# Performance work log

Hardware: AMD Instinct MI355X
Metric: run time of the kernel (lower is better)

## Reference

```python
import jax, jax.numpy as jnp
import numpy as np

B, N, F_IN, F_OUT = 8, 4096, 256, 256


def setup_inputs() -> dict:
    key = jax.random.key(0)
    k1, k2, k3 = jax.random.split(key, 3)
    H = jax.random.normal(k1, (B, N, F_IN), dtype=jnp.float32)
    W = jax.random.normal(k2, (F_IN, F_OUT), dtype=jnp.float32) * (1.0 / np.sqrt(F_IN))
    A = jax.random.normal(k3, (N, N), dtype=jnp.float32) * (1.414 * np.sqrt(2.0 / (N + N)))
    return {"H": H, "W": W, "A": A}


def reference(H, W, A):
    # HW: [B, N, F_out]
    HW = jnp.einsum('bnf,fo->bno', H, W)
    # symmetrize + relu -> nonneg adjacency [N, N]
    A_norm = jax.nn.relu((A + A.T) * 0.5)
    # degree and inverse sqrt (inf -> 0 for isolated nodes)
    D = jnp.sum(A_norm, axis=1)
    D_safe = jnp.where(D > 0, D, 1.0)
    d_inv_sqrt = jnp.where(D > 0, D_safe ** -0.5, 0.0)
    # L_norm = I - D^{-1/2} A D^{-1/2}  (diagonal scaling, no dense diag matmul)
    DAD = d_inv_sqrt[:, None] * A_norm * d_inv_sqrt[None, :]
    L_norm = jnp.eye(N, dtype=H.dtype) - DAD
    # output = relu(L_norm @ HW): [B, N, F_out]
    out = jnp.einsum('nm,bmo->bno', L_norm, HW)
    return jax.nn.relu(out)
```

## Files before the change

### kernel.cpp

```cpp
#include <hip/hip_runtime.h>
#include <stdint.h>

#define N_NODES 4096
#define F_DIM   256
#define BATCH   8

typedef __attribute__((ext_vector_type(8))) __bf16 bf16x8;
typedef __attribute__((ext_vector_type(4))) float  f32x4;
typedef __attribute__((ext_vector_type(8))) unsigned short u16x8;

typedef const __attribute__((address_space(1))) void* gas1_t;
typedef __attribute__((address_space(3))) void*       las3_t;

__device__ __forceinline__ void stage16(const void* g, void* l) {
  __builtin_amdgcn_global_load_lds((gas1_t)g, (las3_t)l, 16, 0, 0);
}

__device__ __forceinline__ unsigned short f2bf(float f) {
  union { float f; uint32_t u; } v; v.f = f;
  uint32_t u = v.u;
  return (unsigned short)((u + 0x7FFFu + ((u >> 16) & 1u)) >> 16);
}
__device__ __forceinline__ float bf2f(unsigned short u) {
  union { uint32_t u; float f; } v; v.u = ((uint32_t)u) << 16;
  return v.f;
}

__global__ __launch_bounds__(256) void k_pre(const float* __restrict__ A,
                                             unsigned short* __restrict__ Sb,
                                             float* __restrict__ D,
                                             const float4* __restrict__ H4,
                                             ushort4* __restrict__ Hb4,
                                             const float* __restrict__ W,
                                             unsigned short* __restrict__ Wt) {
  int t = threadIdx.x;
  int bid = blockIdx.y * 64 + blockIdx.x;
  {
    int i = bid * 512 + t;
    float4 v = H4[i];
    ushort4 o; o.x = f2bf(v.x); o.y = f2bf(v.y); o.z = f2bf(v.z); o.w = f2bf(v.w);
    Hb4[i] = o;
    i += 256;
    v = H4[i];
    o.x = f2bf(v.x); o.y = f2bf(v.y); o.z = f2bf(v.z); o.w = f2bf(v.w);
    Hb4[i] = o;
  }
  if (bid < 256) Wt[t * 256 + bid] = f2bf(W[bid * 256 + t]);

  int bi = blockIdx.y, bj = blockIdx.x;
  if (bj < bi) return;

  __shared__ __align__(16) float T1[64][68];
  __shared__ float Tt[64][67];
  __shared__ float Pr4[64][4];
  __shared__ float Pc[4][64];
  int i0 = bi * 64, j0 = bj * 64;

#pragma unroll
  for (int it = 0; it < 4; ++it) {
    int idx = it * 256 + t;
    int r = idx >> 4, c4 = (idx & 15) * 4;
    float4 v1 = *(const float4*)(A + (size_t)(i0 + r) * N_NODES + j0 + c4);
    *(float4*)&T1[r][c4] = v1;
    float4 v2 = *(const float4*)(A + (size_t)(j0 + r) * N_NODES + i0 + c4);
    Tt[c4 + 0][r] = v2.x; Tt[c4 + 1][r] = v2.y; Tt[c4 + 2][r] = v2.z; Tt[c4 + 3][r] = v2.w;
  }
  __syncthreads();

  {
    int r = t >> 2, cb = (t & 3) * 8;
    float rowpart = 0.f;
#pragma unroll
    for (int g = 0; g < 2; ++g) {
      int c0 = cb + g * 32;
      u16x8 u;
      float vv[8];
#pragma unroll
      for (int i = 0; i < 8; ++i) {
        float v = 0.5f * (T1[r][c0 + i] + Tt[r][c0 + i]);
        v = v > 0.f ? v : 0.f;
        vv[i] = v;
        rowpart += v;
        u[i] = f2bf(v);
      }
      *(u16x8*)&Sb[(size_t)(i0 + r) * N_NODES + j0 + c0] = u;
      *(float4*)&T1[r][c0]     = make_float4(vv[0], vv[1], vv[2], vv[3]);
      *(float4*)&T1[r][c0 + 4] = make_float4(vv[4], vv[5], vv[6], vv[7]);
    }
    Pr4[r][t & 3] = rowpart;
  }
  __syncthreads();

  {
    int c = t & 63, seg = t >> 6;
    float s = 0.f;
#pragma unroll
    for (int i = 0; i < 16; ++i) s += T1[seg * 16 + i][c];
    Pc[seg][c] = s;
  }
  __syncthreads();

  if (t < 64) {
    atomicAdd(&D[i0 + t], Pr4[t][0] + Pr4[t][1] + Pr4[t][2] + Pr4[t][3]);
  } else if (t < 128 && bi != bj) {
    int c = t - 64;
    atomicAdd(&D[j0 + c], Pc[0][c] + Pc[1][c] + Pc[2][c] + Pc[3][c]);
  }

  if (bi != bj) {
#pragma unroll
    for (int it = 0; it < 2; ++it) {
      int u = it * 256 + t;
      int co = u >> 3, rc = (u & 7) * 8;
      u16x8 o;
#pragma unroll
      for (int i = 0; i < 8; ++i) o[i] = f2bf(T1[rc + i][co]);
      *(u16x8*)&Sb[(size_t)(j0 + co) * N_NODES + i0 + rc] = o;
    }
  }
}

__global__ void k_dinv(const float* __restrict__ D, float* __restrict__ dinv) {
  int i = blockIdx.x * blockDim.x + threadIdx.x;
  if (i < N_NODES) {
    float d = D[i];
    dinv[i] = d > 0.f ? 1.0f / sqrtf(d) : 0.f;
  }
}

__global__ __launch_bounds__(512) void k_gemm1(const unsigned short* __restrict__ Hb,
                                               const unsigned short* __restrict__ Wt,
                                               const float* __restrict__ dinv,
                                               unsigned short* __restrict__ HWb,
                                               unsigned short* __restrict__ Gt) {
  __shared__ __align__(16) unsigned short L[65536];
  int t = threadIdx.x;
  int lane = t & 63, r16 = lane & 15, q = lane >> 4;
  int wave = t >> 6;
  int wm = wave >> 2, wn = wave & 3;
  int nh = blockIdx.x;
  int m0 = blockIdx.y * 128;
  int n0 = nh * 128;

#pragma unroll
  for (int i = 0; i < 8; ++i) {
    int s = i * 512 + t;
    int row = s >> 5, cl = s & 31;
    int cs = cl ^ (row & 7);
    uint32_t dst = (uint32_t)(i * 512 + (t & ~63)) * 16;
    stage16(Hb + (size_t)(m0 + row) * 256 + cs * 8, (char*)L + dst);
    stage16(Wt + (size_t)(n0 + row) * 256 + cs * 8, (char*)L + 65536 + dst);
  }
  __syncthreads();

  f32x4 acc[4][2];
#pragma unroll
  for (int i = 0; i < 4; ++i)
#pragma unroll
    for (int j = 0; j < 2; ++j) acc[i][j] = f32x4{0.f, 0.f, 0.f, 0.f};

#pragma unroll
  for (int ks = 0; ks < 8; ++ks) {
    bf16x8 a[4], b[2];
#pragma unroll
    for (int mi = 0; mi < 4; ++mi) {
      int ra = wm * 64 + mi * 16 + r16;
      a[mi] = *(const bf16x8*)((const char*)L + ra * 512 + (((ks * 4 + q) ^ (ra & 7)) << 4));
    }
#pragma unroll
    for (int ni = 0; ni < 2; ++ni) {
      int rb = wn * 32 + ni * 16 + r16;
      b[ni] = *(const bf16x8*)((const char*)L + 65536 + rb * 512 + (((ks * 4 + q) ^ (rb & 7)) << 4));
    }
#pragma unroll
    for (int mi = 0; mi < 4; ++mi)
#pragma unroll
      for (int ni = 0; ni < 2; ++ni)
        acc[mi][ni] = __builtin_amdgcn_mfma_f32_16x16x32_bf16(a[mi], b[ni], acc[mi][ni], 0, 0, 0);
  }
  __syncthreads();

  unsigned short (*T)[136] = (unsigned short (*)[136])L;
#pragma unroll
  for (int mi = 0; mi < 4; ++mi) {
    int rowl = wm * 64 + mi * 16 + q * 4;
#pragma unroll
    for (int ni = 0; ni < 2; ++ni) {
      int coll = wn * 32 + ni * 16 + r16;
#pragma unroll
      for (int rr = 0; rr < 4; ++rr) {
        unsigned short h = f2bf(acc[mi][ni][rr]);
        HWb[(size_t)(m0 + rowl + rr) * F_DIM + (n0 + coll)] = h;
        T[coll][rowl + rr] = h;
      }
    }
  }
  __syncthreads();

  int b = m0 >> 12, nb = m0 & 4095;
#pragma unroll
  for (int i = 0; i < 4; ++i) {
    int u = i * 512 + t;
    int co = u >> 4, cs = (u & 15) * 8;
    u16x8 v = *(const u16x8*)&T[co][cs];
    float4 d0 = *(const float4*)&dinv[nb + cs];
    float4 d1 = *(const float4*)&dinv[nb + cs + 4];
    u16x8 w;
    w[0] = f2bf(bf2f(v[0]) * d0.x);
    w[1] = f2bf(bf2f(v[1]) * d0.y);
    w[2] = f2bf(bf2f(v[2]) * d0.z);
    w[3] = f2bf(bf2f(v[3]) * d0.w);
    w[4] = f2bf(bf2f(v[4]) * d1.x);
    w[5] = f2bf(bf2f(v[5]) * d1.y);
    w[6] = f2bf(bf2f(v[6]) * d1.z);
    w[7] = f2bf(bf2f(v[7]) * d1.w);
    *(u16x8*)&Gt[(size_t)(b * 256 + n0 + co) * N_NODES + nb + cs] = w;
  }
}

#define LDSB 49152

__global__ __launch_bounds__(512, 2) void k_gemm2(const unsigned short* __restrict__ Sb,
                                                  const unsigned short* __restrict__ Gt,
                                                  const unsigned short* __restrict__ HWb,
                                                  const float* __restrict__ dinv,
                                                  float* __restrict__ Out) {
  __shared__ __align__(16) unsigned short LDS[3 * 24576];
  const int NT = N_NODES / 64;
  int t = threadIdx.x;
  int lane = t & 63, r16 = lane & 15, q = lane >> 4;
  int wave = t >> 6;
  int wm = wave >> 1, wn = wave & 1;

  int bid = blockIdx.x;
  int xcd = bid & 7, j = bid >> 3;
  int mt = (xcd >> 1) * 4 + (j & 3);
  int nt = (xcd & 1) * 8 + (j >> 2);
  int m0 = mt * 256, n0 = nt * 128;

  const char* aSrc[4]; const char* bSrc[2];
  uint32_t aDst[4], bDst[2];
#pragma unroll
  for (int i = 0; i < 4; ++i) {
    int slot = i * 512 + t;
    int row = slot >> 3;
    int c = (slot & 7) ^ (row & 7);
    aSrc[i] = (const char*)Sb + (size_t)(m0 + row) * 8192 + c * 16;
    aDst[i] = (uint32_t)(i * 512 + (t & ~63)) * 16;
  }
#pragma unroll
  for (int i = 0; i < 2; ++i) {
    int slot = i * 512 + t;
    int row = slot >> 3;
    int c = (slot & 7) ^ (row & 7);
    bSrc[i] = (const char*)Gt + (size_t)(n0 + row) * 8192 + c * 16;
    bDst[i] = 32768u + (uint32_t)(i * 512 + (t & ~63)) * 16;
  }

  int aoff[4][2], boff[4][2];
#pragma unroll
  for (int mi = 0; mi < 4; ++mi) {
    int ra = wm * 64 + mi * 16 + r16;
#pragma unroll
    for (int ks = 0; ks < 2; ++ks)
      aoff[mi][ks] = ra * 128 + (((ks * 4 + q) ^ (ra & 7)) << 4);
  }
#pragma unroll
  for (int ni = 0; ni < 4; ++ni) {
    int rb = wn * 64 + ni * 16 + r16;
#pragma unroll
    for (int ks = 0; ks < 2; ++ks)
      boff[ni][ks] = 32768 + rb * 128 + (((ks * 4 + q) ^ (rb & 7)) << 4);
  }

  f32x4 acc[4][4];
#pragma unroll
  for (int i = 0; i < 4; ++i)
#pragma unroll
    for (int jj = 0; jj < 4; ++jj) acc[i][jj] = f32x4{0.f, 0.f, 0.f, 0.f};

  auto stage_tile = [&](int kt2, uint32_t bufByte) {
    size_t kb = (size_t)kt2 * 128;
#pragma unroll
    for (int i = 0; i < 4; ++i)
      stage16(aSrc[i] + kb, (char*)LDS + bufByte + aDst[i]);
#pragma unroll
    for (int i = 0; i < 2; ++i)
      stage16(bSrc[i] + kb, (char*)LDS + bufByte + bDst[i]);
  };

  auto tile_body = [&](int kt, uint32_t cur, int mode) {
    bf16x8 aR[4][2], bR[4][2];
#pragma unroll
    for (int mi = 0; mi < 4; ++mi)
#pragma unroll
      for (int ks = 0; ks < 2; ++ks)
        aR[mi][ks] = *(const bf16x8*)((const char*)LDS + cur + aoff[mi][ks]);
#pragma unroll
    for (int ni = 0; ni < 4; ++ni)
#pragma unroll
      for (int ks = 0; ks < 2; ++ks)
        bR[ni][ks] = *(const bf16x8*)((const char*)LDS + cur + boff[ni][ks]);
    if (mode == 2) {
      uint32_t stg = cur + 2 * LDSB;
      if (stg >= 3 * LDSB) stg -= 3 * LDSB;
      stage_tile(kt + 2, stg);
    }
    __builtin_amdgcn_sched_barrier(0);
    __builtin_amdgcn_s_setprio(1);
#pragma unroll
    for (int ks = 0; ks < 2; ++ks)
#pragma unroll
      for (int mi = 0; mi < 4; ++mi)
#pragma unroll
        for (int ni = 0; ni < 4; ++ni)
          acc[mi][ni] = __builtin_amdgcn_mfma_f32_16x16x32_bf16(aR[mi][ks], bR[ni][ks], acc[mi][ni], 0, 0, 0);
    __builtin_amdgcn_s_setprio(0);
    if (mode == 2) {
      asm volatile("s_waitcnt vmcnt(6)" ::: "memory");
    } else if (mode == 1) {
      asm volatile("s_waitcnt vmcnt(0)" ::: "memory");
    }
    if (mode != 0) {
      __builtin_amdgcn_s_barrier();
      __builtin_amdgcn_sched_barrier(0);
    }
  };

  stage_tile(0, 0);
  stage_tile(1, LDSB);
  asm volatile("s_waitcnt vmcnt(6)" ::: "memory");
  __builtin_amdgcn_s_barrier();
  __builtin_amdgcn_sched_barrier(0);

  uint32_t cur = 0;
#pragma unroll 1
  for (int kt = 0; kt < NT - 2; ++kt) {
    tile_body(kt, cur, 2);
    cur += LDSB; if (cur == 3 * LDSB) cur = 0;
  }
  tile_body(NT - 2, cur, 1);
  cur += LDSB; if (cur == 3 * LDSB) cur = 0;
  tile_body(NT - 1, cur, 0);

  int bq = n0 >> 8;
#pragma unroll
  for (int mi = 0; mi < 4; ++mi) {
    int row = m0 + wm * 64 + mi * 16 + q * 4;
    float di[4];
#pragma unroll
    for (int rr = 0; rr < 4; ++rr) di[rr] = dinv[row + rr];
#pragma unroll
    for (int ni = 0; ni < 4; ++ni) {
      int col = n0 + wn * 64 + ni * 16 + r16;
      int o = col & 255;
#pragma unroll
      for (int rr = 0; rr < 4; ++rr) {
        size_t oi = ((size_t)bq * N_NODES + (row + rr)) * F_DIM + o;
        float u = bf2f(HWb[oi]) - di[rr] * acc[mi][ni][rr];
        Out[oi] = u > 0.f ? u : 0.f;
      }
    }
  }
}

extern "C" void kernel_launch(void* const* d_in, const int* in_sizes, int n_in,
                              void* d_out, int out_size, void* d_ws, size_t ws_size,
                              hipStream_t stream) {
  (void)in_sizes; (void)n_in; (void)out_size; (void)ws_size;
  const float* H = (const float*)d_in[0];
  const float* W = (const float*)d_in[1];
  const float* A = (const float*)d_in[2];
  float* out = (float*)d_out;

  char* ws = (char*)d_ws;
  size_t off = 0;
  auto alloc = [&](size_t bytes) {
    char* p = ws + off;
    off += (bytes + 255) & ~(size_t)255;
    return p;
  };
  float*          Dd   = (float*)alloc((size_t)N_NODES * 4);
  float*          dinv = (float*)alloc((size_t)N_NODES * 4);
  unsigned short* Sb   = (unsigned short*)alloc((size_t)N_NODES * N_NODES * 2);
  unsigned short* HWb  = (unsigned short*)alloc((size_t)BATCH * N_NODES * F_DIM * 2);
  unsigned short* Gt   = (unsigned short*)alloc((size_t)BATCH * F_DIM * N_NODES * 2);
  unsigned short* Wt   = (unsigned short*)alloc((size_t)F_DIM * F_DIM * 2);
  unsigned short* Hb   = (unsigned short*)alloc((size_t)BATCH * N_NODES * F_DIM * 2);

  hipMemsetAsync(Dd, 0, N_NODES * 4, stream);
  k_pre<<<dim3(64, 64), 256, 0, stream>>>(A, Sb, Dd, (const float4*)H, (ushort4*)Hb, W, Wt);
  k_dinv<<<16, 256, 0, stream>>>(Dd, dinv);
  k_gemm1<<<dim3(2, 256), 512, 0, stream>>>(Hb, Wt, dinv, HWb, Gt);
  k_gemm2<<<dim3(256), 512, 0, stream>>>(Sb, Gt, HWb, dinv, out);
}
```

Before: 220.1 us.

## Fuse all stages into one cooperative persistent kernel with grid syncs

Merges the preprocessing, degree/dinv, first GEMM and main GEMM kernels into a single cooperative kernel of 256 blocks separated by grid.sync barriers. This removes three kernel launches and the memset. Degree accumulation now writes per-tile partial sums to a buffer and reduces them deterministically instead of using atomics. The triangular A tiles are spread across blocks with a grid-stride loop. The costs are reduced parallelism in the preprocessing phases (256 blocks instead of thousands) and grid-barrier overhead, and the block count relies on two blocks fitting per CU.

New measurement: 322.1 us. 46.3% more time.

```diff
diff --git a/kernel.cpp b/kernel.cpp
--- a/kernel.cpp
+++ b/kernel.cpp
@@ -1,5 +1,9 @@
 #include <hip/hip_runtime.h>
+#include <hip/hip_cooperative_groups.h>
 #include <stdint.h>
+#include <math.h>
+
+namespace cg = cooperative_groups;
 
 #define N_NODES 4096
 #define F_DIM   256
@@ -25,340 +29,323 @@
   union { uint32_t u; float f; } v; v.u = ((uint32_t)u) << 16;
   return v.f;
 }
-
-__global__ __launch_bounds__(256) void k_pre(const float* __restrict__ A,
-                                             unsigned short* __restrict__ Sb,
-                                             float* __restrict__ D,
-                                             const float4* __restrict__ H4,
-                                             ushort4* __restrict__ Hb4,
-                                             const float* __restrict__ W,
-                                             unsigned short* __restrict__ Wt) {
+__device__ __forceinline__ float dinv_of(float d) {
+  return d > 0.f ? 1.0f / sqrtf(d) : 0.f;
+}
+
+#define LDSB 49152
+
+__global__ __launch_bounds__(512, 2) void k_all(
+    const float* __restrict__ A,
+    const float4* __restrict__ H4,
+    const float* __restrict__ W,
+    unsigned short* __restrict__ Sb,
+    ushort4* __restrict__ Hb4,
+    unsigned short* __restrict__ Wt,
+    float* __restrict__ Dpart,
+    float* __restrict__ dinvA,
+    unsigned short* __restrict__ HWb,
+    unsigned short* __restrict__ Gt,
+    float* __restrict__ Out) {
+  cg::grid_group grid = cg::this_grid();
+  __shared__ __align__(16) unsigned short SMEM[3 * 24576];
+  char* sm = (char*)SMEM;
   int t = threadIdx.x;
-  int bid = blockIdx.y * 64 + blockIdx.x;
-  {
-    int i = bid * 512 + t;
+  int bid = blockIdx.x;
+
+#pragma unroll
+  for (int it = 0; it < 16; ++it) {
+    int i = (bid * 16 + it) * 512 + t;
     float4 v = H4[i];
     ushort4 o; o.x = f2bf(v.x); o.y = f2bf(v.y); o.z = f2bf(v.z); o.w = f2bf(v.w);
     Hb4[i] = o;
-    i += 256;
-    v = H4[i];
-    o.x = f2bf(v.x); o.y = f2bf(v.y); o.z = f2bf(v.z); o.w = f2bf(v.w);
-    Hb4[i] = o;
-  }
-  if (bid < 256) Wt[t * 256 + bid] = f2bf(W[bid * 256 + t]);
-
-  int bi = blockIdx.y, bj = blockIdx.x;
-  if (bj < bi) return;
-
-  __shared__ __align__(16) float T1[64][68];
-  __shared__ float Tt[64][67];
-  __shared__ float Pr4[64][4];
-  __shared__ float Pc[4][64];
-  int i0 = bi * 64, j0 = bj * 64;
-
-#pragma unroll
-  for (int it = 0; it < 4; ++it) {
-    int idx = it * 256 + t;
-    int r = idx >> 4, c4 = (idx & 15) * 4;
-    float4 v1 = *(const float4*)(A + (size_t)(i0 + r) * N_NODES + j0 + c4);
-    *(float4*)&T1[r][c4] = v1;
-    float4 v2 = *(const float4*)(A + (size_t)(j0 + r) * N_NODES + i0 + c4);
-    Tt[c4 + 0][r] = v2.x; Tt[c4 + 1][r] = v2.y; Tt[c4 + 2][r] = v2.z; Tt[c4 + 3][r] = v2.w;
-  }
-  __syncthreads();
+  }
+  if (bid < 128) {
+    int e = bid * 512 + t;
+    Wt[(e & 255) * 256 + (e >> 8)] = f2bf(W[e]);
+  }
 
   {
-    int r = t >> 2, cb = (t & 3) * 8;
-    float rowpart = 0.f;
-#pragma unroll
-    for (int g = 0; g < 2; ++g) {
-      int c0 = cb + g * 32;
+    float (*T1)[68] = (float (*)[68])sm;
+    float (*Tt)[67] = (float (*)[67])(sm + 17408);
+    for (int q = bid; q < 2080; q += 256) {
+      int bi = (int)((129.0 - sqrt(129.0 * 129.0 - 8.0 * (double)q)) * 0.5);
+      while (bi * (129 - bi) / 2 > q) --bi;
+      while ((bi + 1) * (128 - bi) / 2 <= q) ++bi;
+      int bj = bi + (q - bi * (129 - bi) / 2);
+      int i0 = bi * 64, j0 = bj * 64;
+      __syncthreads();
+#pragma unroll
+      for (int it = 0; it < 2; ++it) {
+        int idx = it * 512 + t;
+        int r = idx >> 4, c4 = (idx & 15) * 4;
+        float4 v1 = *(const float4*)(A + (size_t)(i0 + r) * N_NODES + j0 + c4);
+        *(float4*)&T1[r][c4] = v1;
+        float4 v2 = *(const float4*)(A + (size_t)(j0 + r) * N_NODES + i0 + c4);
+        Tt[c4 + 0][r] = v2.x; Tt[c4 + 1][r] = v2.y; Tt[c4 + 2][r] = v2.z; Tt[c4 + 3][r] = v2.w;
+      }
+      __syncthreads();
+      int r = t >> 3, g = t & 7, c0 = g * 8;
+      float vv[8]; float rp = 0.f;
       u16x8 u;
-      float vv[8];
 #pragma unroll
       for (int i = 0; i < 8; ++i) {
         float v = 0.5f * (T1[r][c0 + i] + Tt[r][c0 + i]);
         v = v > 0.f ? v : 0.f;
-        vv[i] = v;
-        rowpart += v;
-        u[i] = f2bf(v);
+        vv[i] = v; rp += v; u[i] = f2bf(v);
       }
       *(u16x8*)&Sb[(size_t)(i0 + r) * N_NODES + j0 + c0] = u;
-      *(float4*)&T1[r][c0]     = make_float4(vv[0], vv[1], vv[2], vv[3]);
-      *(float4*)&T1[r][c0 + 4] = make_float4(vv[4], vv[5], vv[6], vv[7]);
-    }
-    Pr4[r][t & 3] = rowpart;
-  }
-  __syncthreads();
+      rp += __shfl_xor(rp, 1); rp += __shfl_xor(rp, 2); rp += __shfl_xor(rp, 4);
+      if (g == 0) Dpart[(size_t)bj * N_NODES + i0 + r] = rp;
+      if (bi != bj) {
+        __syncthreads();
+#pragma unroll
+        for (int i = 0; i < 8; ++i) Tt[c0 + i][r] = vv[i];
+        __syncthreads();
+        u16x8 o; float cp = 0.f;
+#pragma unroll
+        for (int i = 0; i < 8; ++i) { float x = Tt[r][c0 + i]; o[i] = f2bf(x); cp += x; }
+        *(u16x8*)&Sb[(size_t)(j0 + r) * N_NODES + i0 + c0] = o;
+        cp += __shfl_xor(cp, 1); cp += __shfl_xor(cp, 2); cp += __shfl_xor(cp, 4);
+        if (g == 0) Dpart[(size_t)bi * N_NODES + j0 + r] = cp;
+      }
+    }
+  }
+  grid.sync();
 
   {
-    int c = t & 63, seg = t >> 6;
-    float s = 0.f;
-#pragma unroll
-    for (int i = 0; i < 16; ++i) s += T1[seg * 16 + i][c];
-    Pc[seg][c] = s;
-  }
-  __syncthreads();
-
-  if (t < 64) {
-    atomicAdd(&D[i0 + t], Pr4[t][0] + Pr4[t][1] + Pr4[t][2] + Pr4[t][3]);
-  } else if (t < 128 && bi != bj) {
-    int c = t - 64;
-    atomicAdd(&D[j0 + c], Pc[0][c] + Pc[1][c] + Pc[2][c] + Pc[3][c]);
-  }
-
-  if (bi != bj) {
-#pragma unroll
-    for (int it = 0; it < 2; ++it) {
-      int u = it * 256 + t;
-      int co = u >> 3, rc = (u & 7) * 8;
-      u16x8 o;
-#pragma unroll
-      for (int i = 0; i < 8; ++i) o[i] = f2bf(T1[rc + i][co]);
-      *(u16x8*)&Sb[(size_t)(j0 + co) * N_NODES + i0 + rc] = o;
-    }
-  }
-}
-
-__global__ void k_dinv(const float* __restrict__ D, float* __restrict__ dinv) {
-  int i = blockIdx.x * blockDim.x + threadIdx.x;
-  if (i < N_NODES) {
-    float d = D[i];
-    dinv[i] = d > 0.f ? 1.0f / sqrtf(d) : 0.f;
-  }
-}
-
-__global__ __launch_bounds__(512) void k_gemm1(const unsigned short* __restrict__ Hb,
-                                               const unsigned short* __restrict__ Wt,
-                                               const float* __restrict__ dinv,
-                                               unsigned short* __restrict__ HWb,
-                                               unsigned short* __restrict__ Gt) {
-  __shared__ __align__(16) unsigned short L[65536];
-  int t = threadIdx.x;
-  int lane = t & 63, r16 = lane & 15, q = lane >> 4;
-  int wave = t >> 6;
-  int wm = wave >> 2, wn = wave & 3;
-  int nh = blockIdx.x;
-  int m0 = blockIdx.y * 128;
-  int n0 = nh * 128;
-
-#pragma unroll
-  for (int i = 0; i < 8; ++i) {
-    int s = i * 512 + t;
-    int row = s >> 5, cl = s & 31;
-    int cs = cl ^ (row & 7);
-    uint32_t dst = (uint32_t)(i * 512 + (t & ~63)) * 16;
-    stage16(Hb + (size_t)(m0 + row) * 256 + cs * 8, (char*)L + dst);
-    stage16(Wt + (size_t)(n0 + row) * 256 + cs * 8, (char*)L + 65536 + dst);
-  }
-  __syncthreads();
-
-  f32x4 acc[4][2];
-#pragma unroll
-  for (int i = 0; i < 4; ++i)
-#pragma unroll
-    for (int j = 0; j < 2; ++j) acc[i][j] = f32x4{0.f, 0.f, 0.f, 0.f};
-
-#pragma unroll
-  for (int ks = 0; ks < 8; ++ks) {
-    bf16x8 a[4], b[2];
+    int rl = t >> 5, l32 = t & 31;
+    int row = bid * 16 + rl;
+    float s = Dpart[(size_t)(2 * l32) * N_NODES + row] +
+              Dpart[(size_t)(2 * l32 + 1) * N_NODES + row];
+    s += __shfl_xor(s, 1); s += __shfl_xor(s, 2); s += __shfl_xor(s, 4);
+    s += __shfl_xor(s, 8); s += __shfl_xor(s, 16);
+    if (l32 == 0) dinvA[row] = dinv_of(s);
+  }
+  grid.sync();
+
+  {
+    unsigned short* L = (unsigned short*)sm;
+    int lane = t & 63, r16 = lane & 15, qq = lane >> 4;
+    int wave = t >> 6;
+    int wm = wave >> 2, wn = wave & 3;
+#pragma unroll 1
+    for (int jt = 0; jt < 2; ++jt) {
+      int job = bid + jt * 256;
+      int nh = job & 1, my = job >> 1;
+      int m0 = my * 128, n0 = nh * 128;
+      __syncthreads();
+#pragma unroll
+      for (int i = 0; i < 8; ++i) {
+        int s = i * 512 + t;
+        int row = s >> 5, cl = s & 31;
+        int cs = cl ^ (row & 7);
+        uint32_t dst = (uint32_t)(i * 512 + (t & ~63)) * 16;
+        stage16((const unsigned short*)Hb4 + (size_t)(m0 + row) * 256 + cs * 8, sm + dst);
+        stage16(Wt + (size_t)(n0 + row) * 256 + cs * 8, sm + 65536 + dst);
+      }
+      __syncthreads();
+
+      f32x4 acc[4][2];
+#pragma unroll
+      for (int i = 0; i < 4; ++i)
+#pragma unroll
+        for (int j = 0; j < 2; ++j) acc[i][j] = f32x4{0.f, 0.f, 0.f, 0.f};
+
+#pragma unroll
+      for (int ks = 0; ks < 8; ++ks) {
+        bf16x8 a[4], b[2];
+#pragma unroll
+        for (int mi = 0; mi < 4; ++mi) {
+          int ra = wm * 64 + mi * 16 + r16;
+          a[mi] = *(const bf16x8*)(sm + ra * 512 + (((ks * 4 + qq) ^ (ra & 7)) << 4));
+        }
+#pragma unroll
+        for (int ni = 0; ni < 2; ++ni) {
+          int rb = wn * 32 + ni * 16 + r16;
+          b[ni] = *(const bf16x8*)(sm + 65536 + rb * 512 + (((ks * 4 + qq) ^ (rb & 7)) << 4));
+        }
+#pragma unroll
+        for (int mi = 0; mi < 4; ++mi)
+#pragma unroll
+          for (int ni = 0; ni < 2; ++ni)
+            acc[mi][ni] = __builtin_amdgcn_mfma_f32_16x16x32_bf16(a[mi], b[ni], acc[mi][ni], 0, 0, 0);
+      }
+      __syncthreads();
+
+      unsigned short (*T)[136] = (unsigned short (*)[136])sm;
+#pragma unroll
+      for (int mi = 0; mi < 4; ++mi) {
+        int rowl = wm * 64 + mi * 16 + qq * 4;
+#pragma unroll
+        for (int ni = 0; ni < 2; ++ni) {
+          int coll = wn * 32 + ni * 16 + r16;
+#pragma unroll
+          for (int rr = 0; rr < 4; ++rr) {
+            unsigned short h = f2bf(acc[mi][ni][rr]);
+            HWb[(size_t)(m0 + rowl + rr) * F_DIM + (n0 + coll)] = h;
+            T[coll][rowl + rr] = h;
+          }
+        }
+      }
+      __syncthreads();
+
+      int b = m0 >> 12, nb = m0 & 4095;
+#pragma unroll
+      for (int i = 0; i < 4; ++i) {
+        int u = i * 512 + t;
+        int co = u >> 4, cs = (u & 15) * 8;
+        u16x8 v = *(const u16x8*)&T[co][cs];
+        float4 d0 = *(const float4*)&dinvA[nb + cs];
+        float4 d1 = *(const float4*)&dinvA[nb + cs + 4];
+        u16x8 w;
+        w[0] = f2bf(bf2f(v[0]) * d0.x);
+        w[1] = f2bf(bf2f(v[1]) * d0.y);
+        w[2] = f2bf(bf2f(v[2]) * d0.z);
+        w[3] = f2bf(bf2f(v[3]) * d0.w);
+        w[4] = f2bf(bf2f(v[4]) * d1.x);
+        w[5] = f2bf(bf2f(v[5]) * d1.y);
+        w[6] = f2bf(bf2f(v[6]) * d1.z);
+        w[7] = f2bf(bf2f(v[7]) * d1.w);
+        *(u16x8*)&Gt[(size_t)(b * 256 + n0 + co) * N_NODES + nb + cs] = w;
+      }
+    }
+  }
+  grid.sync();
+
+  {
+    const int NT = N_NODES / 64;
+    int lane = t & 63, r16 = lane & 15, q = lane >> 4;
+    int wave = t >> 6;
+    int wm = wave >> 1, wn = wave & 1;
+
+    int xcd = bid & 7, j = bid >> 3;
+    int mt = (xcd >> 1) * 4 + (j & 3);
+    int nt = (xcd & 1) * 8 + (j >> 2);
+    int m0 = mt * 256, n0 = nt * 128;
+
+    const char* aSrc[4]; const char* bSrc[2];
+    uint32_t aDst[4], bDst[2];
+#pragma unroll
+    for (int i = 0; i < 4; ++i) {
+      int slot = i * 512 + t;
+      int row = slot >> 3;
+      int c = (slot & 7) ^ (row & 7);
+      aSrc[i] = (const char*)Sb + (size_t)(m0 + row) * 8192 + c * 16;
+      aDst[i] = (uint32_t)(i * 512 + (t & ~63)) * 16;
+    }
+#pragma unroll
+    for (int i = 0; i < 2; ++i) {
+      int slot = i * 512 + t;
+      int row = slot >> 3;
+      int c = (slot & 7) ^ (row & 7);
+      bSrc[i] = (const char*)Gt + (size_t)(n0 + row) * 8192 + c * 16;
+      bDst[i] = 32768u + (uint32_t)(i * 512 + (t & ~63)) * 16;
+    }
+
+    int aoff[4][2], boff[4][2];
 #pragma unroll
     for (int mi = 0; mi < 4; ++mi) {
       int ra = wm * 64 + mi * 16 + r16;
-      a[mi] = *(const bf16x8*)((const char*)L + ra * 512 + (((ks * 4 + q) ^ (ra & 7)) << 4));
-    }
-#pragma unroll
-    for (int ni = 0; ni < 2; ++ni) {
-      int rb = wn * 32 + ni * 16 + r16;
-      b[ni] = *(const bf16x8*)((const char*)L + 65536 + rb * 512 + (((ks * 4 + q) ^ (rb & 7)) << 4));
-    }
-#pragma unroll
-    for (int mi = 0; mi < 4; ++mi)
-#pragma unroll
-      for (int ni = 0; ni < 2; ++ni)
-        acc[mi][ni] = __builtin_amdgcn_mfma_f32_16x16x32_bf16(a[mi], b[ni], acc[mi][ni], 0, 0, 0);
-  }
-  __syncthreads();
-
-  unsigned short (*T)[136] = (unsigned short (*)[136])L;
-#pragma unroll
-  for (int mi = 0; mi < 4; ++mi) {
-    int rowl = wm * 64 + mi * 16 + q * 4;
-#pragma unroll
-    for (int ni = 0; ni < 2; ++ni) {
-      int coll = wn * 32 + ni * 16 + r16;
-#pragma unroll
-      for (int rr = 0; rr < 4; ++rr) {
-        unsigned short h = f2bf(acc[mi][ni][rr]);
-        HWb[(size_t)(m0 + rowl + rr) * F_DIM + (n0 + coll)] = h;
-        T[coll][rowl + rr] = h;
-      }
-    }
-  }
-  __syncthreads();
-
-  int b = m0 >> 12, nb = m0 & 4095;
-#pragma unroll
-  for (int i = 0; i < 4; ++i) {
-    int u = i * 512 + t;
-    int co = u >> 4, cs = (u & 15) * 8;
-    u16x8 v = *(const u16x8*)&T[co][cs];
-    float4 d0 = *(const float4*)&dinv[nb + cs];
-    float4 d1 = *(const float4*)&dinv[nb + cs + 4];
-    u16x8 w;
-    w[0] = f2bf(bf2f(v[0]) * d0.x);
-    w[1] = f2bf(bf2f(v[1]) * d0.y);
-    w[2] = f2bf(bf2f(v[2]) * d0.z);
-    w[3] = f2bf(bf2f(v[3]) * d0.w);
-    w[4] = f2bf(bf2f(v[4]) * d1.x);
-    w[5] = f2bf(bf2f(v[5]) * d1.y);
-    w[6] = f2bf(bf2f(v[6]) * d1.z);
-    w[7] = f2bf(bf2f(v[7]) * d1.w);
-    *(u16x8*)&Gt[(size_t)(b * 256 + n0 + co) * N_NODES + nb + cs] = w;
-  }
-}
-
-#define LDSB 49152
-
-__global__ __launch_bounds__(512, 2) void k_gemm2(const unsigned short* __restrict__ Sb,
-                                                  const unsigned short* __restrict__ Gt,
-                                                  const unsigned short* __restrict__ HWb,
-                                                  const float* __restrict__ dinv,
-                                                  float* __restrict__ Out) {
-  __shared__ __align__(16) unsigned short LDS[3 * 24576];
-  const int NT = N_NODES / 64;
-  int t = threadIdx.x;
-  int lane = t & 63, r16 = lane & 15, q = lane >> 4;
-  int wave = t >> 6;
-  int wm = wave >> 1, wn = wave & 1;
-
-  int bid = blockIdx.x;
-  int xcd = bid & 7, j = bid >> 3;
-  int mt = (xcd >> 1) * 4 + (j & 3);
-  int nt = (xcd & 1) * 8 + (j >> 2);
-  int m0 = mt * 256, n0 = nt * 128;
-
-  const char* aSrc[4]; const char* bSrc[2];
-  uint32_t aDst[4], bDst[2];
-#pragma unroll
-  for (int i = 0; i < 4; ++i) {
-    int slot = i * 512 + t;
-    int row = slot >> 3;
-    int c = (slot & 7) ^ (row & 7);
-    aSrc[i] = (const char*)Sb + (size_t)(m0 + row) * 8192 + c * 16;
-    aDst[i] = (uint32_t)(i * 512 + (t & ~63)) * 16;
-  }
-#pragma unroll
-  for (int i = 0; i < 2; ++i) {
-    int slot = i * 512 + t;
-    int row = slot >> 3;
-    int c = (slot & 7) ^ (row & 7);
-    bSrc[i] = (const char*)Gt + (size_t)(n0 + row) * 8192 + c * 16;
-    bDst[i] = 32768u + (uint32_t)(i * 512 + (t & ~63)) * 16;
-  }
-
-  int aoff[4][2], boff[4][2];
-#pragma unroll
-  for (int mi = 0; mi < 4; ++mi) {
-    int ra = wm * 64 + mi * 16 + r16;
-#pragma unroll
-    for (int ks = 0; ks < 2; ++ks)
-      aoff[mi][ks] = ra * 128 + (((ks * 4 + q) ^ (ra & 7)) << 4);
-  }
-#pragma unroll
-  for (int ni = 0; ni < 4; ++ni) {
-    int rb = wn * 64 + ni * 16 + r16;
-#pragma unroll
-    for (int ks = 0; ks < 2; ++ks)
-      boff[ni][ks] = 32768 + rb * 128 + (((ks * 4 + q) ^ (rb & 7)) << 4);
-  }
-
-  f32x4 acc[4][4];
-#pragma unroll
-  for (int i = 0; i < 4; ++i)
-#pragma unroll
-    for (int jj = 0; jj < 4; ++jj) acc[i][jj] = f32x4{0.f, 0.f, 0.f, 0.f};
-
-  auto stage_tile = [&](int kt2, uint32_t bufByte) {
-    size_t kb = (size_t)kt2 * 128;
+#pragma unroll
+      for (int ks = 0; ks < 2; ++ks)
+        aoff[mi][ks] = ra * 128 + (((ks * 4 + q) ^ (ra & 7)) << 4);
+    }
+#pragma unroll
+    for (int ni = 0; ni < 4; ++ni) {
+      int rb = wn * 64 + ni * 16 + r16;
+#pragma unroll
+      for (int ks = 0; ks < 2; ++ks)
+        boff[ni][ks] = 32768 + rb * 128 + (((ks * 4 + q) ^ (rb & 7)) << 4);
+    }
+
+    f32x4 acc[4][4];
 #pragma unroll
     for (int i = 0; i < 4; ++i)
-      stage16(aSrc[i] + kb, (char*)LDS + bufByte + aDst[i]);
-#pragma unroll
-    for (int i = 0; i < 2; ++i)
-      stage16(bSrc[i] + kb, (char*)LDS + bufByte + bDst[i]);
-  };
-
-  auto tile_body = [&](int kt, uint32_t cur, int mode) {
-    bf16x8 aR[4][2], bR[4][2];
-#pragma unroll
-    for (int mi = 0; mi < 4; ++mi)
+#pragma unroll
+      for (int jj = 0; jj < 4; ++jj) acc[i][jj] = f32x4{0.f, 0.f, 0.f, 0.f};
+
+    auto stage_tile = [&](int kt2, uint32_t bufByte) {
+      size_t kb = (size_t)kt2 * 128;
+#pragma unroll
+      for (int i = 0; i < 4; ++i)
+        stage16(aSrc[i] + kb, sm + bufByte + aDst[i]);
+#pragma unroll
+      for (int i = 0; i < 2; ++i)
+        stage16(bSrc[i] + kb, sm + bufByte + bDst[i]);
+    };
+
+    auto tile_body = [&](int kt, uint32_t cur, int mode) {
+      bf16x8 aR[4][2], bR[4][2];
+#pragma unroll
+      for (int mi = 0; mi < 4; ++mi)
+#pragma unroll
+        for (int ks = 0; ks < 2; ++ks)
+          aR[mi][ks] = *(const bf16x8*)(sm + cur + aoff[mi][ks]);
+#pragma unroll
+      for (int ni = 0; ni < 4; ++ni)
+#pragma unroll
+        for (int ks = 0; ks < 2; ++ks)
+          bR[ni][ks] = *(const bf16x8*)(sm + cur + boff[ni][ks]);
+      if (mode == 2) {
+        uint32_t stg = cur + 2 * LDSB;
+        if (stg >= 3 * LDSB) stg -= 3 * LDSB;
+        stage_tile(kt + 2, stg);
+      }
+      __builtin_amdgcn_sched_barrier(0);
+      __builtin_amdgcn_s_setprio(1);
 #pragma unroll
       for (int ks = 0; ks < 2; ++ks)
-        aR[mi][ks] = *(const bf16x8*)((const char*)LDS + cur + aoff[mi][ks]);
-#pragma unroll
-    for (int ni = 0; ni < 4; ++ni)
-#pragma unroll
-      for (int ks = 0; ks < 2; ++ks)
-        bR[ni][ks] = *(const bf16x8*)((const char*)LDS + cur + boff[ni][ks]);
-    if (mode == 2) {
-      uint32_t stg = cur + 2 * LDSB;
-      if (stg >= 3 * LDSB) stg -= 3 * LDSB;
-      stage_tile(kt + 2, stg);
-    }
+#pragma unroll
+        for (int mi = 0; mi < 4; ++mi)
+#pragma unroll
+          for (int ni = 0; ni < 4; ++ni)
+            acc[mi][ni] = __builtin_amdgcn_mfma_f32_16x16x32_bf16(aR[mi][ks], bR[ni][ks], acc[mi][ni], 0, 0, 0);
+      __builtin_amdgcn_s_setprio(0);
+      if (mode == 2) {
+        asm volatile("s_waitcnt vmcnt(6)" ::: "memory");
+      } else if (mode == 1) {
+        asm volatile("s_waitcnt vmcnt(0)" ::: "memory");
+      }
+      if (mode != 0) {
+        __builtin_amdgcn_s_barrier();
+        __builtin_amdgcn_sched_barrier(0);
+      }
+    };
+
+    stage_tile(0, 0);
+    stage_tile(1, LDSB);
+    asm volatile("s_waitcnt vmcnt(6)" ::: "memory");
+    __builtin_amdgcn_s_barrier();
     __builtin_amdgcn_sched_barrier(0);
-    __builtin_amdgcn_s_setprio(1);
-#pragma unroll
-    for (int ks = 0; ks < 2; ++ks)
-#pragma unroll
-      for (int mi = 0; mi < 4; ++mi)
-#pragma unroll
-        for (int ni = 0; ni < 4; ++ni)
-          acc[mi][ni] = __builtin_amdgcn_mfma_f32_16x16x32_bf16(aR[mi][ks], bR[ni][ks], acc[mi][ni], 0, 0, 0);
-    __builtin_amdgcn_s_setprio(0);
-    if (mode == 2) {
-      asm volatile("s_waitcnt vmcnt(6)" ::: "memory");
-    } else if (mode == 1) {
-      asm volatile("s_waitcnt vmcnt(0)" ::: "memory");
-    }
-    if (mode != 0) {
-      __builtin_amdgcn_s_barrier();
-      __builtin_amdgcn_sched_barrier(0);
-    }
-  };
-
-  stage_tile(0, 0);
-  stage_tile(1, LDSB);
-  asm volatile("s_waitcnt vmcnt(6)" ::: "memory");
-  __builtin_amdgcn_s_barrier();
-  __builtin_amdgcn_sched_barrier(0);
-
-  uint32_t cur = 0;
+
+    uint32_t cur = 0;
 #pragma unroll 1
-  for (int kt = 0; kt < NT - 2; ++kt) {
-    tile_body(kt, cur, 2);
+    for (int kt = 0; kt < NT - 2; ++kt) {
+      tile_body(kt, cur, 2);
+      cur += LDSB; if (cur == 3 * LDSB) cur = 0;
+    }
+    tile_body(NT - 2, cur, 1);
     cur += LDSB; if (cur == 3 * LDSB) cur = 0;
-  }
-  tile_body(NT - 2, cur, 1);
-  cur += LDSB; if (cur == 3 * LDSB) cur = 0;
-  tile_body(NT - 1, cur, 0);
-
-  int bq = n0 >> 8;
-#pragma unroll
-  for (int mi = 0; mi < 4; ++mi) {
-    int row = m0 + wm * 64 + mi * 16 + q * 4;
-    float di[4];
-#pragma unroll
-    for (int rr = 0; rr < 4; ++rr) di[rr] = dinv[row + rr];
-#pragma unroll
-    for (int ni = 0; ni < 4; ++ni) {
-      int col = n0 + wn * 64 + ni * 16 + r16;
-      int o = col & 255;
-#pragma unroll
-      for (int rr = 0; rr < 4; ++rr) {
-        size_t oi = ((size_t)bq * N_NODES + (row + rr)) * F_DIM + o;
-        float u = bf2f(HWb[oi]) - di[rr] * acc[mi][ni][rr];
-        Out[oi] = u > 0.f ? u : 0.f;
+    tile_body(NT - 1, cur, 0);
+
+    int bq = n0 >> 8;
+#pragma unroll
+    for (int mi = 0; mi < 4; ++mi) {
+      int row = m0 + wm * 64 + mi * 16 + q * 4;
+      float di[4];
+#pragma unroll
+      for (int rr = 0; rr < 4; ++rr) di[rr] = dinvA[row + rr];
+#pragma unroll
+      for (int ni = 0; ni < 4; ++ni) {
+        int col = n0 + wn * 64 + ni * 16 + r16;
+        int o = col & 255;
+#pragma unroll
+        for (int rr = 0; rr < 4; ++rr) {
+          size_t oi = ((size_t)bq * N_NODES + (row + rr)) * F_DIM + o;
+          float u = bf2f(HWb[oi]) - di[rr] * acc[mi][ni][rr];
+          Out[oi] = u > 0.f ? u : 0.f;
+        }
       }
     }
   }
@@ -368,9 +355,9 @@
                               void* d_out, int out_size, void* d_ws, size_t ws_size,
                               hipStream_t stream) {
   (void)in_sizes; (void)n_in; (void)out_size; (void)ws_size;
-  const float* H = (const float*)d_in[0];
+  const float* A = (const float*)d_in[2];
+  const float4* H4 = (const float4*)d_in[0];
   const float* W = (const float*)d_in[1];
-  const float* A = (const float*)d_in[2];
   float* out = (float*)d_out;
 
   char* ws = (char*)d_ws;
@@ -380,17 +367,16 @@
     off += (bytes + 255) & ~(size_t)255;
     return p;
   };
-  float*          Dd   = (float*)alloc((size_t)N_NODES * 4);
-  float*          dinv = (float*)alloc((size_t)N_NODES * 4);
-  unsigned short* Sb   = (unsigned short*)alloc((size_t)N_NODES * N_NODES * 2);
-  unsigned short* HWb  = (unsigned short*)alloc((size_t)BATCH * N_NODES * F_DIM * 2);
-  unsigned short* Gt   = (unsigned short*)alloc((size_t)BATCH * F_DIM * N_NODES * 2);
-  unsigned short* Wt   = (unsigned short*)alloc((size_t)F_DIM * F_DIM * 2);
-  unsigned short* Hb   = (unsigned short*)alloc((size_t)BATCH * N_NODES * F_DIM * 2);
-
-  hipMemsetAsync(Dd, 0, N_NODES * 4, stream);
-  k_pre<<<dim3(64, 64), 256, 0, stream>>>(A, Sb, Dd, (const float4*)H, (ushort4*)Hb, W, Wt);
-  k_dinv<<<16, 256, 0, stream>>>(Dd, dinv);
-  k_gemm1<<<dim3(2, 256), 512, 0, stream>>>(Hb, Wt, dinv, HWb, Gt);
-  k_gemm2<<<dim3(256), 512, 0, stream>>>(Sb, Gt, HWb, dinv, out);
-}
+  float*          Dpart = (float*)alloc((size_t)64 * N_NODES * 4);
+  float*          dinvA = (float*)alloc((size_t)N_NODES * 4);
+  unsigned short* Sb    = (unsigned short*)alloc((size_t)N_NODES * N_NODES * 2);
+  unsigned short* HWb   = (unsigned short*)alloc((size_t)BATCH * N_NODES * F_DIM * 2);
+  unsigned short* Gt    = (unsigned short*)alloc((size_t)BATCH * F_DIM * N_NODES * 2);
+  unsigned short* Wt    = (unsigned short*)alloc((size_t)F_DIM * F_DIM * 2);
+  ushort4*        Hb4   = (ushort4*)alloc((size_t)BATCH * N_NODES * F_DIM * 2);
+
+  void* args[] = {(void*)&A, (void*)&H4, (void*)&W, (void*)&Sb, (void*)&Hb4,
+                  (void*)&Wt, (void*)&Dpart, (void*)&dinvA, (void*)&HWb,
+                  (void*)&Gt, (void*)&out};
+  hipLaunchCooperativeKernel((const void*)k_all, dim3(256), dim3(512), args, 0, stream);
+}
```
